# Kernel tuning notes

Hardware: AMD Instinct MI355X
Metric: run time of the kernel (lower is better)

Reference implementation:

```python
import jax, jax.numpy as jnp
import numpy as np

EMBED_DIM = 1024
NUM_HEADS = 16
HEAD_DIM = EMBED_DIM // NUM_HEADS
SCALE = HEAD_DIM ** -0.5


def setup_inputs() -> dict:
    key = jax.random.key(0)
    ks = jax.random.split(key, 9)
    B, S, E = 2, 2048, EMBED_DIM
    std = E ** -0.5
    return {
        "x": jax.random.normal(ks[0], (B, S, E), dtype=jnp.float32),
        "Wq": jax.random.normal(ks[1], (E, E), dtype=jnp.float32) * std,
        "bq": jax.random.normal(ks[2], (E,), dtype=jnp.float32) * 0.01,
        "Wk": jax.random.normal(ks[3], (E, E), dtype=jnp.float32) * std,
        "bk": jax.random.normal(ks[4], (E,), dtype=jnp.float32) * 0.01,
        "Wv": jax.random.normal(ks[5], (E, E), dtype=jnp.float32) * std,
        "bv": jax.random.normal(ks[6], (E,), dtype=jnp.float32) * 0.01,
        "Wo": jax.random.normal(ks[7], (E, E), dtype=jnp.float32) * std,
        "bo": jax.random.normal(ks[8], (E,), dtype=jnp.float32) * 0.01,
    }


def reference(x, Wq, bq, Wk, bk, Wv, bv, Wo, bo):
    B, S, E = x.shape
    H, D = NUM_HEADS, HEAD_DIM
    # torch Linear: y = x @ W.T + b
    q = (x @ Wq.T + bq).reshape(B, S, H, D).transpose(0, 2, 1, 3)  # [B,H,S,D]
    k = (x @ Wk.T + bk).reshape(B, S, H, D).transpose(0, 2, 1, 3)
    v = (x @ Wv.T + bv).reshape(B, S, H, D).transpose(0, 2, 1, 3)
    attn = jnp.einsum("bhqd,bhkd->bhqk", q, k) * SCALE  # [B,H,S,S]
    # NOTE: original code softmaxes over dim=1 (the heads axis) — faithful repro.
    attn = jax.nn.softmax(attn.astype(jnp.float32), axis=1).astype(q.dtype)
    out = jnp.einsum("bhqk,bhkd->bhqd", attn, v)  # [B,H,S,D]
    out = out.transpose(0, 2, 1, 3).reshape(B, S, E)
    out = out @ Wo.T + bo
    return out, attn
```

## Files before the change

kernel.cpp:

```cpp
#include <hip/hip_runtime.h>

typedef _Float16 hf2 __attribute__((ext_vector_type(2)));
typedef _Float16 hf4 __attribute__((ext_vector_type(4)));
typedef _Float16 hf8 __attribute__((ext_vector_type(8)));
typedef float    fx4 __attribute__((ext_vector_type(4)));

#define GLD16(gp, lp) __builtin_amdgcn_global_load_lds(                      \
    (const __attribute__((address_space(1))) void*)(gp),                     \
    (__attribute__((address_space(3))) void*)(lp), 16, 0, 0)

__global__ __launch_bounds__(256) void cvt_x_k(const float* __restrict__ s,
                                               _Float16* __restrict__ d) {
  size_t i = (size_t)blockIdx.x * 256 + threadIdx.x;
  float4 v = ((const float4*)s)[i];
  hf4 o = {(_Float16)v.x, (_Float16)v.y, (_Float16)v.z, (_Float16)v.w};
  *(hf4*)(d + 4 * i) = o;
}

__global__ __launch_bounds__(256) void cvt_w_k(const float* __restrict__ s0,
                                               const float* __restrict__ s1,
                                               const float* __restrict__ s2,
                                               const float* __restrict__ s3,
                                               _Float16* __restrict__ d) {
  const float* s = blockIdx.y == 0 ? s0 : blockIdx.y == 1 ? s1 : blockIdx.y == 2 ? s2 : s3;
  size_t i = (size_t)blockIdx.x * 256 + threadIdx.x;
  float4 v = ((const float4*)s)[i];
  hf4 o = {(_Float16)v.x, (_Float16)v.y, (_Float16)v.z, (_Float16)v.w};
  *(hf4*)(d + (size_t)blockIdx.y * 1048576 + 4 * i) = o;
}

__device__ __forceinline__ void gemm_tile(
    const _Float16* __restrict__ A, const _Float16* __restrict__ B,
    const float* __restrict__ bias, _Float16* __restrict__ Ch,
    float* __restrict__ Cf, int m0, int n0, int ldc, int mode)
{
  __shared__ alignas(16) _Float16 Asm[2][128 * 32];
  __shared__ alignas(16) _Float16 Bsm[2][128 * 32];
  const int tid = (int)threadIdx.x;
  const int lane = tid & 63, wv = tid >> 6;
  const int col = lane & 15, g = lane >> 4;

  fx4 acc[2][8];
#pragma unroll
  for (int i = 0; i < 2; ++i)
#pragma unroll
    for (int j = 0; j < 8; ++j) acc[i][j] = fx4{0.f, 0.f, 0.f, 0.f};

  const int cp0 = tid, cp1 = tid + 256;
  const int row0 = cp0 >> 2, row1 = cp1 >> 2;
  const int ch0 = (cp0 & 3) ^ ((row0 >> 1) & 3);
  const int ch1 = (cp1 & 3) ^ ((row1 >> 1) & 3);
  const _Float16* a0 = A + (size_t)(m0 + row0) * 1024 + ch0 * 8;
  const _Float16* a1 = A + (size_t)(m0 + row1) * 1024 + ch1 * 8;
  const _Float16* b0 = B + (size_t)(n0 + row0) * 1024 + ch0 * 8;
  const _Float16* b1 = B + (size_t)(n0 + row1) * 1024 + ch1 * 8;

  int aoff[2], boff[8];
#pragma unroll
  for (int mi = 0; mi < 2; ++mi) {
    int row = wv * 32 + mi * 16 + col;
    aoff[mi] = (row * 4 + (g ^ ((row >> 1) & 3))) * 8;
  }
#pragma unroll
  for (int nj = 0; nj < 8; ++nj) {
    int row = nj * 16 + col;
    boff[nj] = (row * 4 + (g ^ ((row >> 1) & 3))) * 8;
  }

#define STAGE_T(bufi, kt) {                          \
    GLD16(a0 + (kt) * 32, &Asm[bufi][cp0 * 8]);      \
    GLD16(a1 + (kt) * 32, &Asm[bufi][cp1 * 8]);      \
    GLD16(b0 + (kt) * 32, &Bsm[bufi][cp0 * 8]);      \
    GLD16(b1 + (kt) * 32, &Bsm[bufi][cp1 * 8]); }

  STAGE_T(0, 0);
  int buf = 0;
  for (int kt = 0; kt < 32; ++kt) {
    __syncthreads();
    if (kt + 1 < 32) STAGE_T(buf ^ 1, kt + 1);
    hf8 af[2], bf[8];
#pragma unroll
    for (int mi = 0; mi < 2; ++mi) af[mi] = *(const hf8*)&Asm[buf][aoff[mi]];
#pragma unroll
    for (int nj = 0; nj < 8; ++nj) bf[nj] = *(const hf8*)&Bsm[buf][boff[nj]];
#pragma unroll
    for (int mi = 0; mi < 2; ++mi)
#pragma unroll
      for (int nj = 0; nj < 8; ++nj)
        acc[mi][nj] = __builtin_amdgcn_mfma_f32_16x16x32_f16(af[mi], bf[nj], acc[mi][nj], 0, 0, 0);
    buf ^= 1;
  }
#undef STAGE_T

  if (mode == 2) {
#pragma unroll
    for (int nj = 0; nj < 8; ++nj) {
      float bn = bias[n0 + nj * 16 + col];
#pragma unroll
      for (int mi = 0; mi < 2; ++mi)
#pragma unroll
        for (int r = 0; r < 4; ++r)
          Cf[(size_t)(m0 + wv * 32 + mi * 16 + 4 * g + r) * ldc + n0 + nj * 16 + col] =
              acc[mi][nj][r] + bn;
    }
  } else if (mode == 0) {
#pragma unroll
    for (int nj = 0; nj < 8; ++nj) {
      float bn = bias[n0 + nj * 16 + col];
#pragma unroll
      for (int mi = 0; mi < 2; ++mi)
#pragma unroll
        for (int r = 0; r < 4; ++r)
          Ch[(size_t)(m0 + wv * 32 + mi * 16 + 4 * g + r) * ldc + n0 + nj * 16 + col] =
              (_Float16)(acc[mi][nj][r] + bn);
    }
  } else {
#pragma unroll
    for (int mi = 0; mi < 2; ++mi)
#pragma unroll
      for (int r = 0; r < 4; ++r) {
        float bm = bias[m0 + wv * 32 + mi * 16 + 4 * g + r];
#pragma unroll
        for (int nj = 0; nj < 8; ++nj)
          Ch[(size_t)(m0 + wv * 32 + mi * 16 + 4 * g + r) * ldc + n0 + nj * 16 + col] =
              (_Float16)(acc[mi][nj][r] + bm);
      }
  }
}

__global__ __launch_bounds__(256, 3) void qkv_gemm_k(
    const _Float16* __restrict__ xh, const _Float16* __restrict__ Wqh,
    const _Float16* __restrict__ Wkh, const _Float16* __restrict__ Wvh,
    const float* __restrict__ bq, const float* __restrict__ bk,
    const float* __restrict__ bv, _Float16* __restrict__ Qh,
    _Float16* __restrict__ Kh, _Float16* __restrict__ Vt)
{
  int id = (int)blockIdx.x;
  if (id < 512) {
    int t = id & 255;
    const _Float16* Bp = (id < 256) ? Wqh : Wkh;
    const float*    bp = (id < 256) ? bq : bk;
    _Float16*       Cp = (id < 256) ? Qh : Kh;
    gemm_tile(xh, Bp, bp, Cp, nullptr, (t >> 3) * 128, (t & 7) * 128, 1024, 0);
  } else {
    int t = id - 512;
    gemm_tile(Wvh, xh, bv, Vt, nullptr, (t >> 5) * 128, (t & 31) * 128, 4096, 1);
  }
}

__global__ __launch_bounds__(256, 3) void out_gemm_k(
    const _Float16* __restrict__ Oh, const _Float16* __restrict__ Woh,
    const float* __restrict__ bo, float* __restrict__ outp)
{
  int id = (int)blockIdx.x;
  gemm_tile(Oh, Woh, bo, nullptr, outp, (id >> 3) * 128, (id & 7) * 128, 1024, 2);
}

__global__ __launch_bounds__(256) void repack_v_k(const _Float16* __restrict__ Vt,
                                                  _Float16* __restrict__ V2) {
  const int tid = (int)threadIdx.x;
  const int kgi = (int)blockIdx.x;
  const int h = (int)blockIdx.y, b = (int)blockIdx.z;
  const int k0 = kgi * 128;
  __shared__ alignas(16) _Float16 Vl[64 * 128];
#pragma unroll
  for (int i = 0; i < 4; ++i) {
    int s = tid + i * 256;
    int er = s >> 4, c = s & 15;
    GLD16(Vt + (size_t)(h * 64 + er) * 4096 + b * 2048 + k0 + ((c ^ (er & 15)) * 8),
          Vl + s * 8);
  }
  __syncthreads();
  const int lane = tid & 63, dtsub = tid >> 6;
  const int col = lane & 15, g = lane >> 4;
  const int er = dtsub * 16 + col;
  _Float16* out = V2 + ((((size_t)(b * 16 + h) * 128 + (k0 >> 4)) * 4 + dtsub) * 256) + lane * 4;
#pragma unroll
  for (int ks = 0; ks < 8; ++ks) {
    int cl = 2 * ks + (g >> 1);
    int phys = cl ^ col;
    hf4 v = *(const hf4*)&Vl[er * 128 + phys * 8 + (g & 1) * 4];
    *(hf4*)(out + (size_t)ks * 1024) = v;
  }
}

__global__ __launch_bounds__(256, 4) void qk_stats_k(
    const _Float16* __restrict__ Qh, const _Float16* __restrict__ Kh,
    float* __restrict__ C0, float* __restrict__ C1)
{
  const int tid = (int)threadIdx.x;
  const int lane = tid & 63, wv = tid >> 6;
  const int col = lane & 15, g = lane >> 4;
  const int id = (int)blockIdx.x;
  const int xcd = id & 7, j = id >> 3;
  const int b = xcd >> 2, qq = xcd & 3;
  const int kx = j >> 5, qyl = j & 31;
  const int q0 = (qq * 32 + qyl) * 16;
  const int kt0 = kx * 64;

  __shared__ alignas(16) _Float16 Kt[2][8192];
  __shared__ alignas(16) _Float16 Qt[2][2048];

  const _Float16* Kbase = Kh + (size_t)(b * 2048 + kt0) * 1024;
  const _Float16* Qbase = Qh + (size_t)(b * 2048 + q0) * 1024;

#define STG1(bufi, hp) {                                                      \
    _Pragma("unroll")                                                         \
    for (int i_ = 0; i_ < 4; ++i_) {                                          \
      int s_ = tid + i_ * 256, r_ = s_ >> 4, pc_ = s_ & 15;                   \
      GLD16(Kbase + (size_t)r_ * 1024 + (hp) * 128 + ((pc_ ^ (r_ & 15)) * 8), \
            &Kt[bufi][s_ * 8]);                                               \
    }                                                                         \
    { int r_ = tid >> 4, pc_ = tid & 15;                                      \
      GLD16(Qbase + (size_t)r_ * 1024 + (hp) * 128 + ((pc_ ^ r_) * 8),        \
            &Qt[bufi][tid * 8]); } }

  fx4 lg[16];
#pragma unroll
  for (int h = 0; h < 16; ++h) lg[h] = fx4{0.f, 0.f, 0.f, 0.f};

  STG1(0, 0);
  int buf = 0;
  const int krow = wv * 16 + col;
#pragma unroll
  for (int hp = 0; hp < 8; ++hp) {
    __syncthreads();
    if (hp < 7) STG1(buf ^ 1, hp + 1);
#pragma unroll
    for (int hh = 0; hh < 2; ++hh) {
      const int h = 2 * hp + hh;
      hf8 ka0 = *(const hf8*)&Kt[buf][krow * 128 + (((hh * 8 + 0 + g) ^ (krow & 15)) * 8)];
      hf8 ka1 = *(const hf8*)&Kt[buf][krow * 128 + (((hh * 8 + 4 + g) ^ (krow & 15)) * 8)];
      hf8 qa0 = *(const hf8*)&Qt[buf][col * 128 + (((hh * 8 + 0 + g) ^ col) * 8)];
      hf8 qa1 = *(const hf8*)&Qt[buf][col * 128 + (((hh * 8 + 4 + g) ^ col) * 8)];
      lg[h] = __builtin_amdgcn_mfma_f32_16x16x32_f16(ka0, qa0, lg[h], 0, 0, 0);
      lg[h] = __builtin_amdgcn_mfma_f32_16x16x32_f16(ka1, qa1, lg[h], 0, 0, 0);
    }
    buf ^= 1;
  }
#undef STG1

  fx4 mx = lg[0];
#pragma unroll
  for (int h = 1; h < 16; ++h)
#pragma unroll
    for (int r = 0; r < 4; ++r) mx[r] = fmaxf(mx[r], lg[h][r]);
  fx4 sm = fx4{0.f, 0.f, 0.f, 0.f};
#pragma unroll
  for (int h = 0; h < 16; ++h)
#pragma unroll
    for (int r = 0; r < 4; ++r) sm[r] += __expf((lg[h][r] - mx[r]) * 0.125f);
  fx4 C;
#pragma unroll
  for (int r = 0; r < 4; ++r) C[r] = mx[r] * 0.125f + __logf(sm[r]);

  float* Cb = b ? C1 : C0;
  const int ktp = kx * 4 + wv;
  const int qt  = qq * 32 + qyl;
  *(fx4*)(Cb + ((size_t)ktp * 128 + qt) * 256 + lane * 4) = C;
}

__global__ __launch_bounds__(512, 4) void pv_attn_k(
    const _Float16* __restrict__ Qh, const _Float16* __restrict__ Kh,
    const _Float16* __restrict__ V2, const float* __restrict__ C0,
    const float* __restrict__ C1, float* __restrict__ attnp,
    _Float16* __restrict__ Oh)
{
  const int tid = (int)threadIdx.x;
  const int lane = tid & 63, wv = tid >> 6;
  const int col = lane & 15, g = lane >> 4;
  const int id = (int)blockIdx.x;
  const int lin = (id & 7) * 128 + (id >> 3);
  const int b = lin >> 9, qt64 = (lin >> 4) & 31, h = lin & 15;
  const int q0 = qt64 * 64;

  __shared__ alignas(16) _Float16 Kt[2][8192];
  __shared__ alignas(16) _Float16 Qt[4096];
  __shared__ alignas(16) float    sst[4][16][136];

  const _Float16* Kbh = Kh + (size_t)(b * 2048) * 1024 + h * 64;
  const float*    Cb  = b ? C1 : C0;

#define STGK2(bufi, kc) {                                                     \
    int r0_ = tid >> 3, c0_ = tid & 7;                                        \
    int r1_ = (tid + 512) >> 3, c1_ = (tid + 512) & 7;                        \
    GLD16(Kbh + (size_t)((kc) * 128 + r0_) * 1024 + (c0_ ^ (r0_ & 7)) * 8,    \
          &Kt[bufi][tid * 8]);                                                \
    GLD16(Kbh + (size_t)((kc) * 128 + r1_) * 1024 + (c1_ ^ (r1_ & 7)) * 8,    \
          &Kt[bufi][(tid + 512) * 8]); }

  {
    int qr_ = tid >> 3, qc_ = tid & 7;
    GLD16(Qh + (size_t)(b * 2048 + q0 + qr_) * 1024 + h * 64 + (qc_ ^ (qr_ & 7)) * 8,
          &Qt[tid * 8]);
  }

  fx4 acc[4][4];
#pragma unroll
  for (int t = 0; t < 4; ++t)
#pragma unroll
    for (int dt = 0; dt < 4; ++dt) acc[t][dt] = fx4{0.f, 0.f, 0.f, 0.f};

  STGK2(0, 0);
  int buf = 0;
  const int krow = wv * 16 + col;
  const int srow = 2 * wv + (lane >> 5);
  const int sks  = (lane & 31) * 4;
  float* attnbase = attnp + (size_t)((b * 16 + h) * 2048 + q0) * 2048;
  const _Float16* v2h = V2 + (size_t)(b * 16 + h) * 131072 + lane * 4;

  for (int kc = 0; kc < 16; ++kc) {
    __syncthreads();
    if (kc < 15) STGK2(buf ^ 1, kc + 1);

    hf8 ka0 = *(const hf8*)&Kt[buf][krow * 64 + ((0 + g) ^ (krow & 7)) * 8];
    hf8 ka1 = *(const hf8*)&Kt[buf][krow * 64 + ((4 + g) ^ (krow & 7)) * 8];

    const int ksg = kc * 8 + wv;
    const _Float16* v2b = v2h + (size_t)ksg * 1024;
    hf4 vb[4];
#pragma unroll
    for (int dt = 0; dt < 4; ++dt) vb[dt] = *(const hf4*)(v2b + dt * 256);

#pragma unroll
    for (int t = 0; t < 4; ++t) {
      const int qrow = t * 16 + col;
      hf8 qa0 = *(const hf8*)&Qt[qrow * 64 + ((0 + g) ^ (qrow & 7)) * 8];
      hf8 qa1 = *(const hf8*)&Qt[qrow * 64 + ((4 + g) ^ (qrow & 7)) * 8];
      fx4 lg = fx4{0.f, 0.f, 0.f, 0.f};
      lg = __builtin_amdgcn_mfma_f32_16x16x32_f16(ka0, qa0, lg, 0, 0, 0);
      lg = __builtin_amdgcn_mfma_f32_16x16x32_f16(ka1, qa1, lg, 0, 0, 0);

      fx4 cc = *(const fx4*)(Cb + ((size_t)ksg * 128 + qt64 * 4 + t) * 256 + lane * 4);
      fx4 av;
#pragma unroll
      for (int r = 0; r < 4; ++r) av[r] = __expf(lg[r] * 0.125f - cc[r]);

      hf4 pa = {(_Float16)av[0], (_Float16)av[1], (_Float16)av[2], (_Float16)av[3]};
#pragma unroll
      for (int dt = 0; dt < 4; ++dt)
        acc[t][dt] = __builtin_amdgcn_mfma_f32_16x16x16f16(pa, vb[dt], acc[t][dt], 0, 0, 0);

      *(fx4*)&sst[t][col][wv * 16 + 4 * g] = av;
    }
    __syncthreads();

#pragma unroll
    for (int t = 0; t < 4; ++t) {
      fx4 val = *(const fx4*)&sst[t][srow][sks];
      __builtin_nontemporal_store(
          val, (fx4*)(attnbase + (size_t)(t * 16 + srow) * 2048 + kc * 128 + sks));
    }
    buf ^= 1;
  }
#undef STGK2

  float* Osum = &sst[0][0][0];
  for (int w = 0; w < 8; ++w) {
    __syncthreads();
    if (wv == w) {
#pragma unroll
      for (int t = 0; t < 4; ++t)
#pragma unroll
        for (int dt = 0; dt < 4; ++dt)
#pragma unroll
          for (int r = 0; r < 4; ++r) {
            int idx = (t * 16 + 4 * g + r) * 64 + dt * 16 + col;
            Osum[idx] = (w == 0) ? acc[t][dt][r] : Osum[idx] + acc[t][dt][r];
          }
    }
  }
  __syncthreads();
#pragma unroll
  for (int it = 0; it < 2; ++it) {
    int s = tid + it * 512;
    int q = s >> 4, e4 = (s & 15) * 4;
    hf4 o = {(_Float16)Osum[q * 64 + e4],     (_Float16)Osum[q * 64 + e4 + 1],
             (_Float16)Osum[q * 64 + e4 + 2], (_Float16)Osum[q * 64 + e4 + 3]};
    *(hf4*)(Oh + (size_t)(b * 2048 + q0 + q) * 1024 + h * 64 + e4) = o;
  }
}

extern "C" void kernel_launch(void* const* d_in, const int* in_sizes, int n_in,
                              void* d_out, int out_size, void* d_ws, size_t ws_size,
                              hipStream_t stream) {
  (void)in_sizes; (void)n_in; (void)out_size; (void)ws_size;
  const float* x  = (const float*)d_in[0];
  const float* Wq = (const float*)d_in[1];
  const float* bq = (const float*)d_in[2];
  const float* Wk = (const float*)d_in[3];
  const float* bk = (const float*)d_in[4];
  const float* Wv = (const float*)d_in[5];
  const float* bv = (const float*)d_in[6];
  const float* Wo = (const float*)d_in[7];
  const float* bo = (const float*)d_in[8];

  char* ws = (char*)d_ws;
  _Float16* xh   = (_Float16*)(ws + (0ull  << 20));
  _Float16* V2   = (_Float16*)(ws + (0ull  << 20));
  _Float16* Wqh  = (_Float16*)(ws + (8ull  << 20));
  _Float16* Wkh  = (_Float16*)(ws + (10ull << 20));
  _Float16* Wvh  = (_Float16*)(ws + (12ull << 20));
  _Float16* Woh  = (_Float16*)(ws + (14ull << 20));
  _Float16* Qh   = (_Float16*)(ws + (16ull << 20));
  _Float16* Kh   = (_Float16*)(ws + (24ull << 20));
  _Float16* Vt   = (_Float16*)(ws + (32ull << 20));
  _Float16* Oh   = (_Float16*)(ws + (40ull << 20));
  float*    C1   = (float*)   (ws + (48ull << 20));

  float* outp  = (float*)d_out;
  float* C0    = outp;
  float* attnp = outp + 4194304ull;

  cvt_x_k<<<4096, 256, 0, stream>>>(x, xh);
  cvt_w_k<<<dim3(1024, 4), 256, 0, stream>>>(Wq, Wk, Wv, Wo, Wqh);
  qkv_gemm_k<<<768, 256, 0, stream>>>(xh, Wqh, Wkh, Wvh, bq, bk, bv, Qh, Kh, Vt);
  repack_v_k<<<dim3(16, 16, 2), 256, 0, stream>>>(Vt, V2);
  qk_stats_k<<<8192, 256, 0, stream>>>(Qh, Kh, C0, C1);
  pv_attn_k<<<1024, 512, 0, stream>>>(Qh, Kh, V2, C0, C1, attnp, Oh);
  out_gemm_k<<<256, 256, 0, stream>>>(Oh, Woh, bo, outp);
}
```

Before: 294.8 us.

## Give each wave its own K rows and double-buffer fp16 score staging

Each wave now loads only the 16 K rows it consumes, so the K tile no longer needs a block-wide barrier at the top of every iteration. The barrier is dropped and a single initial sync is added before the loop. The LDS staging buffer for the probabilities written to the attn output becomes fp16 and is double-buffered by iteration parity, which halves staging traffic and makes the removed barrier safe. In exchange, the attention probabilities written out are now fp16-rounded values widened back to float, which lowers output precision.

```diff
diff --git a/kernel.cpp b/kernel.cpp
--- a/kernel.cpp
+++ b/kernel.cpp
@@ -276,24 +276,27 @@
 
   __shared__ alignas(16) _Float16 Kt[2][8192];
   __shared__ alignas(16) _Float16 Qt[4096];
-  __shared__ alignas(16) float    sst[4][16][136];
+  __shared__ alignas(16) _Float16 ssth[2][4][16][136];
 
   const _Float16* Kbh = Kh + (size_t)(b * 2048) * 1024 + h * 64;
   const float*    Cb  = b ? C1 : C0;
 
-#define STGK2(bufi, kc) {                                                     \
-    int r0_ = tid >> 3, c0_ = tid & 7;                                        \
-    int r1_ = (tid + 512) >> 3, c1_ = (tid + 512) & 7;                        \
-    GLD16(Kbh + (size_t)((kc) * 128 + r0_) * 1024 + (c0_ ^ (r0_ & 7)) * 8,    \
-          &Kt[bufi][tid * 8]);                                                \
-    GLD16(Kbh + (size_t)((kc) * 128 + r1_) * 1024 + (c1_ ^ (r1_ & 7)) * 8,    \
-          &Kt[bufi][(tid + 512) * 8]); }
+#define STGKW(bufi, kc) {                                                       \
+    int s0_ = lane, s1_ = lane + 64;                                            \
+    GLD16(Kbh + (size_t)((kc) * 128 + wv * 16 + (s0_ >> 3)) * 1024 +            \
+              ((s0_ & 7) ^ ((s0_ >> 3) & 7)) * 8,                               \
+          &Kt[bufi][wv * 1024 + s0_ * 8]);                                      \
+    GLD16(Kbh + (size_t)((kc) * 128 + wv * 16 + (s1_ >> 3)) * 1024 +            \
+              ((s1_ & 7) ^ ((s1_ >> 3) & 7)) * 8,                               \
+          &Kt[bufi][wv * 1024 + s1_ * 8]); }
 
   {
     int qr_ = tid >> 3, qc_ = tid & 7;
     GLD16(Qh + (size_t)(b * 2048 + q0 + qr_) * 1024 + h * 64 + (qc_ ^ (qr_ & 7)) * 8,
           &Qt[tid * 8]);
   }
+  STGKW(0, 0);
+  __syncthreads();
 
   fx4 acc[4][4];
 #pragma unroll
@@ -301,20 +304,16 @@
 #pragma unroll
     for (int dt = 0; dt < 4; ++dt) acc[t][dt] = fx4{0.f, 0.f, 0.f, 0.f};
 
-  STGK2(0, 0);
   int buf = 0;
-  const int krow = wv * 16 + col;
   const int srow = 2 * wv + (lane >> 5);
   const int sks  = (lane & 31) * 4;
   float* attnbase = attnp + (size_t)((b * 16 + h) * 2048 + q0) * 2048;
   const _Float16* v2h = V2 + (size_t)(b * 16 + h) * 131072 + lane * 4;
 
   for (int kc = 0; kc < 16; ++kc) {
-    __syncthreads();
-    if (kc < 15) STGK2(buf ^ 1, kc + 1);
-
-    hf8 ka0 = *(const hf8*)&Kt[buf][krow * 64 + ((0 + g) ^ (krow & 7)) * 8];
-    hf8 ka1 = *(const hf8*)&Kt[buf][krow * 64 + ((4 + g) ^ (krow & 7)) * 8];
+    hf8 ka0 = *(const hf8*)&Kt[buf][wv * 1024 + col * 64 + ((0 + g) ^ (col & 7)) * 8];
+    hf8 ka1 = *(const hf8*)&Kt[buf][wv * 1024 + col * 64 + ((4 + g) ^ (col & 7)) * 8];
+    if (kc < 15) STGKW(buf ^ 1, kc + 1);
 
     const int ksg = kc * 8 + wv;
     const _Float16* v2b = v2h + (size_t)ksg * 1024;
@@ -341,21 +340,22 @@
       for (int dt = 0; dt < 4; ++dt)
         acc[t][dt] = __builtin_amdgcn_mfma_f32_16x16x16f16(pa, vb[dt], acc[t][dt], 0, 0, 0);
 
-      *(fx4*)&sst[t][col][wv * 16 + 4 * g] = av;
+      *(hf4*)&ssth[kc & 1][t][col][wv * 16 + 4 * g] = pa;
     }
     __syncthreads();
 
 #pragma unroll
     for (int t = 0; t < 4; ++t) {
-      fx4 val = *(const fx4*)&sst[t][srow][sks];
+      hf4 v = *(const hf4*)&ssth[kc & 1][t][srow][sks];
+      fx4 val = {(float)v[0], (float)v[1], (float)v[2], (float)v[3]};
       __builtin_nontemporal_store(
           val, (fx4*)(attnbase + (size_t)(t * 16 + srow) * 2048 + kc * 128 + sks));
     }
     buf ^= 1;
   }
-#undef STGK2
-
-  float* Osum = &sst[0][0][0];
+#undef STGKW
+
+  float* Osum = (float*)&ssth[0][0][0][0];
   for (int w = 0; w < 8; ++w) {
     __syncthreads();
     if (wv == w) {
```

Result: no change. 289.3 us, median of 2 (-1.9%).
